# Optimization experiments

Measured on AMD Instinct MI355X. Metric: run time of the kernel, lower is better.

Reference implementation:

```python
import jax, jax.numpy as jnp
import numpy as np

V, D, H, B, M, T, PAD = 32000, 512, 3, 32, 512, 4, 1


def setup_inputs() -> dict:
    key = jax.random.key(0)
    ks = jax.random.split(key, 10)
    def emb_tables(k):
        t = 0.1 * jax.random.normal(k, (H + 1, V, D), jnp.float32)
        return t.at[:, PAD, :].set(0.0)  # padding_idx rows are zero
    C_enc = emb_tables(ks[0])
    C_dec = emb_tables(ks[1])
    gru_w_ih = 0.1 * jax.random.normal(ks[2], (3 * D, D), jnp.float32)
    gru_w_hh = 0.1 * jax.random.normal(ks[3], (3 * D, D), jnp.float32)
    gru_b_ih = jnp.zeros((3 * D,), jnp.float32)
    gru_b_hh = jnp.zeros((3 * D,), jnp.float32)
    W1_w = 0.1 * jax.random.normal(ks[4], (V, 2 * D), jnp.float32)
    W1_b = jnp.zeros((V,), jnp.float32)
    story = jax.random.randint(ks[5], (B, M, T), 0, V, jnp.int32)
    enc_query = jax.random.randint(ks[6], (B,), 0, V, jnp.int32)
    return {"story": story, "enc_query": enc_query, "C_enc": C_enc,
            "C_dec": C_dec, "gru_w_ih": gru_w_ih, "gru_w_hh": gru_w_hh,
            "gru_b_ih": gru_b_ih, "gru_b_hh": gru_b_hh, "W1_w": W1_w,
            "W1_b": W1_b}


def _mem_embed(table, story):
    # table [V, D], story [B, M, T] -> sum-pooled memory [B, M, D]
    return jnp.sum(table[story], axis=2)


def _forward(C_enc, C_dec, gru_w_ih, gru_w_hh, gru_b_ih, gru_b_hh,
             W1_w, W1_b, story, enc_query):
    # ---- EncoderMemNN.forward (eval mode, no unk_mask dropout) ----
    u = jnp.zeros((story.shape[0], D), C_enc.dtype)
    for hop in range(H):
        m_A = _mem_embed(C_enc[hop], story)            # [B, M, D]
        prob = jax.nn.softmax(jnp.einsum('bmd,bd->bm', m_A, u), axis=1)
        m_C = _mem_embed(C_enc[hop + 1], story)        # [B, M, D]
        u = u + jnp.einsum('bmd,bm->bd', m_C, prob)
    enc_hidden = u                                     # decoder_hidden[0]

    # ---- DecoderrMemNN.ptrMemDecoder: single GRU step ----
    x = C_dec[0][enc_query]                            # [B, D]
    gi = x @ gru_w_ih.T + gru_b_ih                     # [B, 3D]
    gh = enc_hidden @ gru_w_hh.T + gru_b_hh            # [B, 3D]
    i_r, i_z, i_n = jnp.split(gi, 3, axis=1)
    h_r, h_z, h_n = jnp.split(gh, 3, axis=1)
    r = jax.nn.sigmoid(i_r + h_r)
    z = jax.nn.sigmoid(i_z + h_z)
    n = jnp.tanh(i_n + r * h_n)
    hidden = (1.0 - z) * n + z * enc_hidden            # new GRU hidden [B, D]

    # ---- DecoderrMemNN.load_memory: m_story[h] = sum-pooled C_dec[h] ----
    m_story = [_mem_embed(C_dec[h], story) for h in range(H + 1)]

    # ---- multi-hop pointer attention ----
    u0 = hidden
    uk = hidden
    p_vocab = None
    for hop in range(H):
        prob_lg = jnp.einsum('bmd,bd->bm', m_story[hop], uk)   # [B, M]
        prob = jax.nn.softmax(prob_lg, axis=1)
        o_k = jnp.einsum('bmd,bm->bd', m_story[hop + 1], prob)  # [B, D]
        if hop == 0:
            p_vocab = jnp.concatenate([u0, o_k], axis=1) @ W1_w.T + W1_b
        uk = uk + o_k
    p_ptr = prob_lg                                    # logits from last hop
    return p_ptr, p_vocab, hidden[None]                # hidden [1, B, D]


def reference(story, enc_query, C_enc, C_dec, gru_w_ih, gru_w_hh,
              gru_b_ih, gru_b_hh, W1_w, W1_b):
    return _forward(C_enc, C_dec, gru_w_ih, gru_w_hh, gru_b_ih, gru_b_hh,
                    W1_w, W1_b, story, enc_query)
```

## Files before the change

kernel.cpp:

```cpp
#include <hip/hip_runtime.h>
#include <math.h>

#define DD 512
#define MM 512
#define BB 32
#define TT 4
#define VV 32000

__global__ __launch_bounds__(256) void poolwsum_kernel(const float* __restrict__ table,
                                                       const int* __restrict__ story,
                                                       const float* __restrict__ s,
                                                       float* __restrict__ partial) {
  __shared__ float wsh[16];
  __shared__ int rows[64];
  __shared__ float red[16];
  int b = blockIdx.x >> 5;
  int c = blockIdx.x & 31;
  int t = threadIdx.x;
  if (s) {
    float v0 = s[b * MM + t], v1 = s[b * MM + t + 256];
    float mx = fmaxf(v0, v1);
#pragma unroll
    for (int off = 32; off > 0; off >>= 1) mx = fmaxf(mx, __shfl_xor(mx, off));
    if ((t & 63) == 0) red[t >> 6] = mx;
    __syncthreads();
    mx = fmaxf(fmaxf(red[0], red[1]), fmaxf(red[2], red[3]));
    float e0 = expf(v0 - mx), e1 = expf(v1 - mx);
    float sm = e0 + e1;
#pragma unroll
    for (int off = 32; off > 0; off >>= 1) sm += __shfl_xor(sm, off);
    if ((t & 63) == 0) red[8 + (t >> 6)] = sm;
    __syncthreads();
    sm = red[8] + red[9] + red[10] + red[11];
    float inv = 1.0f / sm;
    if (t < 16) wsh[t] = expf(s[b * MM + c * 16 + t] - mx) * inv;
  } else {
    if (t < 16) wsh[t] = 1.0f / MM;
  }
  if (t < 64) rows[t] = story[((b << 9) + (c << 4)) * TT + t];
  __syncthreads();
  float acc0 = 0.f, acc1 = 0.f;
#pragma unroll 8
  for (int i = 0; i < 64; ++i) {
    const float* r = table + (size_t)rows[i] * DD;
    float wm = wsh[i >> 2];
    acc0 += wm * r[t];
    acc1 += wm * r[t + 256];
  }
  float* pp = partial + (size_t)blockIdx.x * DD;
  pp[t] = acc0;
  pp[t + 256] = acc1;
}

__global__ void wsumB_kernel(const float* __restrict__ partial,
                             const float* __restrict__ prev,
                             float* __restrict__ uout) {
  int i = blockIdx.x * 256 + threadIdx.x;
  int b = i >> 9, d = i & 511;
  float acc = prev ? prev[i] : 0.f;
  const float* pp = partial + (size_t)b * 32 * DD + d;
#pragma unroll
  for (int c = 0; c < 32; ++c) acc += pp[c * DD];
  uout[i] = acc;
}

__global__ void wsumB2_kernel(const float* __restrict__ partial,
                              const float* __restrict__ hid,
                              float* __restrict__ uk, float* __restrict__ hc) {
  int i = blockIdx.x * 256 + threadIdx.x;
  int b = i >> 9, d = i & 511;
  float ov = 0.f;
  const float* pp = partial + (size_t)b * 32 * DD + d;
#pragma unroll
  for (int c = 0; c < 32; ++c) ov += pp[c * DD];
  float hv = hid[i];
  uk[i] = hv + ov;
  hc[b * 1024 + d] = hv;
  hc[b * 1024 + 512 + d] = ov;
}

__global__ __launch_bounds__(256) void pooldot_kernel(const float* __restrict__ table,
                                                      const int* __restrict__ story,
                                                      const float* __restrict__ u,
                                                      float* __restrict__ s) {
  int wave = (blockIdx.x << 2) + (threadIdx.x >> 6);
  int lane = threadIdx.x & 63;
  int b = wave >> 9;
  const int* st = story + wave * TT;
  size_t r0 = (size_t)st[0] * DD, r1 = (size_t)st[1] * DD;
  size_t r2 = (size_t)st[2] * DD, r3 = (size_t)st[3] * DD;
  const float4* t4 = (const float4*)table;
  const float4* ur = (const float4*)(u + (size_t)b * DD);
  float acc = 0.f;
#pragma unroll
  for (int h = 0; h < 2; ++h) {
    int c = (h << 6) + lane;
    float4 a = t4[(r0 >> 2) + c];
    float4 bb = t4[(r1 >> 2) + c];
    float4 cc = t4[(r2 >> 2) + c];
    float4 d = t4[(r3 >> 2) + c];
    float4 q = ur[c];
    acc += (a.x + bb.x + cc.x + d.x) * q.x;
    acc += (a.y + bb.y + cc.y + d.y) * q.y;
    acc += (a.z + bb.z + cc.z + d.z) * q.z;
    acc += (a.w + bb.w + cc.w + d.w) * q.w;
  }
#pragma unroll
  for (int off = 32; off > 0; off >>= 1) acc += __shfl_xor(acc, off);
  if (lane == 0) s[wave] = acc;
}

__global__ __launch_bounds__(256) void matvec_kernel(const float* __restrict__ W,
                                                     const float* __restrict__ bias,
                                                     const float* __restrict__ vin,
                                                     const int* __restrict__ q,
                                                     const float* __restrict__ table,
                                                     float* __restrict__ out) {
  int idx = (blockIdx.x << 2) + (threadIdx.x >> 6);
  int lane = threadIdx.x & 63;
  int b = idx / 1536;
  int j = idx - b * 1536;
  const float* xb = vin ? (vin + (size_t)b * DD) : (table + (size_t)q[b] * DD);
  const float4* Wr = (const float4*)(W + (size_t)j * DD);
  const float4* xr = (const float4*)xb;
  float acc = 0.f;
#pragma unroll
  for (int h = 0; h < 2; ++h) {
    int c = (h << 6) + lane;
    float4 a = Wr[c];
    float4 qv = xr[c];
    acc += a.x * qv.x + a.y * qv.y + a.z * qv.z + a.w * qv.w;
  }
#pragma unroll
  for (int off = 32; off > 0; off >>= 1) acc += __shfl_xor(acc, off);
  if (lane == 0) out[idx] = acc + bias[j];
}

__global__ void gate_kernel(const float* __restrict__ gi, const float* __restrict__ gh,
                            const float* __restrict__ u, float* __restrict__ hidden,
                            float* __restrict__ out_h) {
  int i = blockIdx.x * 256 + threadIdx.x;
  int b = i >> 9, d = i & 511;
  const float* gib = gi + b * 1536;
  const float* ghb = gh + b * 1536;
  float i_r = gib[d], i_z = gib[d + 512], i_n = gib[d + 1024];
  float h_r = ghb[d], h_z = ghb[d + 512], h_n = ghb[d + 1024];
  float r = 1.f / (1.f + expf(-(i_r + h_r)));
  float z = 1.f / (1.f + expf(-(i_z + h_z)));
  float n = tanhf(i_n + r * h_n);
  float h = (1.f - z) * n + z * u[i];
  hidden[i] = h;
  out_h[i] = h;
}

__global__ __launch_bounds__(256) void pvocab_kernel(const float* __restrict__ Hcat,
                                                     const float* __restrict__ W1,
                                                     const float* __restrict__ W1b,
                                                     float* __restrict__ out) {
  __shared__ float As[32][36];
  __shared__ float Bs[32][68];
  int t = threadIdx.x;
  int v0 = blockIdx.x * 64;
  int tb = t >> 5;
  int tv = t & 31;
  int br = t >> 2;
  int bk = (t & 3) << 3;
  const float* Wp = W1 + (size_t)(v0 + br) * 1024 + bk;
  int ab = t >> 3;
  int ak = (t & 7) << 2;
  const float* Ap = Hcat + (size_t)ab * 1024 + ak;

  float acc[4][2] = {{0.f, 0.f}, {0.f, 0.f}, {0.f, 0.f}, {0.f, 0.f}};

  float4 aReg = *(const float4*)(Ap);
  float4 wReg0 = *(const float4*)(Wp);
  float4 wReg1 = *(const float4*)(Wp + 4);

  for (int k0 = 0; k0 < 1024; k0 += 32) {
    As[ak + 0][ab] = aReg.x; As[ak + 1][ab] = aReg.y;
    As[ak + 2][ab] = aReg.z; As[ak + 3][ab] = aReg.w;
    Bs[bk + 0][br] = wReg0.x; Bs[bk + 1][br] = wReg0.y;
    Bs[bk + 2][br] = wReg0.z; Bs[bk + 3][br] = wReg0.w;
    Bs[bk + 4][br] = wReg1.x; Bs[bk + 5][br] = wReg1.y;
    Bs[bk + 6][br] = wReg1.z; Bs[bk + 7][br] = wReg1.w;
    __syncthreads();
    if (k0 + 32 < 1024) {
      aReg = *(const float4*)(Ap + k0 + 32);
      wReg0 = *(const float4*)(Wp + k0 + 32);
      wReg1 = *(const float4*)(Wp + k0 + 36);
    }
#pragma unroll
    for (int k = 0; k < 32; ++k) {
      float2 bv = *(const float2*)&Bs[k][tv * 2];
      float4 av = *(const float4*)&As[k][tb * 4];
      acc[0][0] += av.x * bv.x; acc[0][1] += av.x * bv.y;
      acc[1][0] += av.y * bv.x; acc[1][1] += av.y * bv.y;
      acc[2][0] += av.z * bv.x; acc[2][1] += av.z * bv.y;
      acc[3][0] += av.w * bv.x; acc[3][1] += av.w * bv.y;
    }
    __syncthreads();
  }
  int v = v0 + tv * 2;
  float b0 = W1b[v], b1 = W1b[v + 1];
#pragma unroll
  for (int i = 0; i < 4; ++i) {
    float2 r;
    r.x = acc[i][0] + b0;
    r.y = acc[i][1] + b1;
    *(float2*)(out + (size_t)(tb * 4 + i) * VV + v) = r;
  }
}

extern "C" void kernel_launch(void* const* d_in, const int* in_sizes, int n_in,
                              void* d_out, int out_size, void* d_ws, size_t ws_size,
                              hipStream_t stream) {
  const int* story = (const int*)d_in[0];
  const int* q = (const int*)d_in[1];
  const float* C_enc = (const float*)d_in[2];
  const float* C_dec = (const float*)d_in[3];
  const float* W_ih = (const float*)d_in[4];
  const float* W_hh = (const float*)d_in[5];
  const float* b_ih = (const float*)d_in[6];
  const float* b_hh = (const float*)d_in[7];
  const float* W1 = (const float*)d_in[8];
  const float* W1b = (const float*)d_in[9];
  float* out = (float*)d_out;

  const size_t VD = (size_t)VV * DD;
  const float* C1 = C_enc + 1 * VD;
  const float* C2 = C_enc + 2 * VD;
  const float* C3 = C_enc + 3 * VD;
  const float* D0 = C_dec + 0 * VD;
  const float* D1 = C_dec + 1 * VD;
  const float* D2 = C_dec + 2 * VD;

  float* part = (float*)d_ws;
  float* u = part + (size_t)BB * 32 * DD;
  float* s = u + BB * DD;
  float* gi = s + BB * MM;
  float* gh = gi + BB * 3 * DD;
  float* hid = gh + BB * 3 * DD;
  float* uk = hid + BB * DD;
  float* hc = uk + BB * DD;

  float* p_ptr_out = out;
  float* p_vocab_out = out + BB * MM;
  float* hid_out = out + BB * MM + (size_t)BB * VV;

  dim3 blk(256);
  const int pwGrid = BB * 32;
  const int pdGrid = BB * MM / 4;
  const int mvGrid = BB * 3 * DD / 4;
  const int ewGrid = BB * DD / 256;

  poolwsum_kernel<<<pwGrid, blk, 0, stream>>>(C1, story, nullptr, part);
  wsumB_kernel<<<ewGrid, blk, 0, stream>>>(part, nullptr, u);
  pooldot_kernel<<<pdGrid, blk, 0, stream>>>(C1, story, u, s);
  poolwsum_kernel<<<pwGrid, blk, 0, stream>>>(C2, story, s, part);
  wsumB_kernel<<<ewGrid, blk, 0, stream>>>(part, u, u);
  pooldot_kernel<<<pdGrid, blk, 0, stream>>>(C2, story, u, s);
  poolwsum_kernel<<<pwGrid, blk, 0, stream>>>(C3, story, s, part);
  wsumB_kernel<<<ewGrid, blk, 0, stream>>>(part, u, u);

  matvec_kernel<<<mvGrid, blk, 0, stream>>>(W_ih, b_ih, nullptr, q, C_dec, gi);
  matvec_kernel<<<mvGrid, blk, 0, stream>>>(W_hh, b_hh, u, nullptr, nullptr, gh);
  gate_kernel<<<ewGrid, blk, 0, stream>>>(gi, gh, u, hid, hid_out);

  pooldot_kernel<<<pdGrid, blk, 0, stream>>>(D0, story, hid, s);
  poolwsum_kernel<<<pwGrid, blk, 0, stream>>>(D1, story, s, part);
  wsumB2_kernel<<<ewGrid, blk, 0, stream>>>(part, hid, uk, hc);
  pooldot_kernel<<<pdGrid, blk, 0, stream>>>(D1, story, uk, s);
  poolwsum_kernel<<<pwGrid, blk, 0, stream>>>(D2, story, s, part);
  wsumB_kernel<<<ewGrid, blk, 0, stream>>>(part, uk, uk);
  pooldot_kernel<<<pdGrid, blk, 0, stream>>>(D2, story, uk, p_ptr_out);

  pvocab_kernel<<<VV / 64, blk, 0, stream>>>(hc, W1, W1b, p_vocab_out);
}
```

Before: 297.7 us.

## Replace gathered pool-dot with dense vocab dot product plus index gather

Instead of gathering four table rows per memory slot and dotting each with the query, the code computes the query against every vocabulary row as a small tiled GEMM, then sums four scalar lookups per slot. This turns random 2KB row gathers (about twice the table size per call) into a single coalesced streaming pass over the table. It adds a 32x32000 intermediate buffer and an extra kernel launch per hop, and the GEMM grid of 500 blocks may leave some CUs idle.

```diff
diff --git a/kernel.cpp b/kernel.cpp
--- a/kernel.cpp
+++ b/kernel.cpp
@@ -79,35 +79,70 @@
   hc[b * 1024 + 512 + d] = ov;
 }
 
-__global__ __launch_bounds__(256) void pooldot_kernel(const float* __restrict__ table,
-                                                      const int* __restrict__ story,
-                                                      const float* __restrict__ u,
-                                                      float* __restrict__ s) {
-  int wave = (blockIdx.x << 2) + (threadIdx.x >> 6);
-  int lane = threadIdx.x & 63;
-  int b = wave >> 9;
-  const int* st = story + wave * TT;
-  size_t r0 = (size_t)st[0] * DD, r1 = (size_t)st[1] * DD;
-  size_t r2 = (size_t)st[2] * DD, r3 = (size_t)st[3] * DD;
-  const float4* t4 = (const float4*)table;
-  const float4* ur = (const float4*)(u + (size_t)b * DD);
-  float acc = 0.f;
-#pragma unroll
-  for (int h = 0; h < 2; ++h) {
-    int c = (h << 6) + lane;
-    float4 a = t4[(r0 >> 2) + c];
-    float4 bb = t4[(r1 >> 2) + c];
-    float4 cc = t4[(r2 >> 2) + c];
-    float4 d = t4[(r3 >> 2) + c];
-    float4 q = ur[c];
-    acc += (a.x + bb.x + cc.x + d.x) * q.x;
-    acc += (a.y + bb.y + cc.y + d.y) * q.y;
-    acc += (a.z + bb.z + cc.z + d.z) * q.z;
-    acc += (a.w + bb.w + cc.w + d.w) * q.w;
-  }
-#pragma unroll
-  for (int off = 32; off > 0; off >>= 1) acc += __shfl_xor(acc, off);
-  if (lane == 0) s[wave] = acc;
+__global__ __launch_bounds__(256) void dotV_kernel(const float* __restrict__ u,
+                                                   const float* __restrict__ C,
+                                                   float* __restrict__ dotv) {
+  __shared__ float As[32][36];
+  __shared__ float Bs[32][68];
+  int t = threadIdx.x;
+  int v0 = blockIdx.x * 64;
+  int tb = t >> 5;
+  int tv = t & 31;
+  int br = t >> 2;
+  int bk = (t & 3) << 3;
+  const float* Wp = C + (size_t)(v0 + br) * DD + bk;
+  int ab = t >> 3;
+  int ak = (t & 7) << 2;
+  const float* Ap = u + (size_t)ab * DD + ak;
+
+  float acc[4][2] = {{0.f, 0.f}, {0.f, 0.f}, {0.f, 0.f}, {0.f, 0.f}};
+
+  float4 aReg = *(const float4*)(Ap);
+  float4 wReg0 = *(const float4*)(Wp);
+  float4 wReg1 = *(const float4*)(Wp + 4);
+
+  for (int k0 = 0; k0 < DD; k0 += 32) {
+    As[ak + 0][ab] = aReg.x; As[ak + 1][ab] = aReg.y;
+    As[ak + 2][ab] = aReg.z; As[ak + 3][ab] = aReg.w;
+    Bs[bk + 0][br] = wReg0.x; Bs[bk + 1][br] = wReg0.y;
+    Bs[bk + 2][br] = wReg0.z; Bs[bk + 3][br] = wReg0.w;
+    Bs[bk + 4][br] = wReg1.x; Bs[bk + 5][br] = wReg1.y;
+    Bs[bk + 6][br] = wReg1.z; Bs[bk + 7][br] = wReg1.w;
+    __syncthreads();
+    if (k0 + 32 < DD) {
+      aReg = *(const float4*)(Ap + k0 + 32);
+      wReg0 = *(const float4*)(Wp + k0 + 32);
+      wReg1 = *(const float4*)(Wp + k0 + 36);
+    }
+#pragma unroll
+    for (int k = 0; k < 32; ++k) {
+      float2 bv = *(const float2*)&Bs[k][tv * 2];
+      float4 av = *(const float4*)&As[k][tb * 4];
+      acc[0][0] += av.x * bv.x; acc[0][1] += av.x * bv.y;
+      acc[1][0] += av.y * bv.x; acc[1][1] += av.y * bv.y;
+      acc[2][0] += av.z * bv.x; acc[2][1] += av.z * bv.y;
+      acc[3][0] += av.w * bv.x; acc[3][1] += av.w * bv.y;
+    }
+    __syncthreads();
+  }
+  int v = v0 + tv * 2;
+#pragma unroll
+  for (int i = 0; i < 4; ++i) {
+    float2 r;
+    r.x = acc[i][0];
+    r.y = acc[i][1];
+    *(float2*)(dotv + (size_t)(tb * 4 + i) * VV + v) = r;
+  }
+}
+
+__global__ void gatherS_kernel(const float* __restrict__ dotv,
+                               const int* __restrict__ story,
+                               float* __restrict__ out) {
+  int i = blockIdx.x * 256 + threadIdx.x;
+  int b = i >> 9;
+  const float* dv = dotv + (size_t)b * VV;
+  int4 ix = *(const int4*)(story + (size_t)i * 4);
+  out[i] = dv[ix.x] + dv[ix.y] + dv[ix.z] + dv[ix.w];
 }
 
 __global__ __launch_bounds__(256) void matvec_kernel(const float* __restrict__ W,
@@ -235,7 +270,8 @@
   const float* D2 = C_dec + 2 * VD;
 
   float* part = (float*)d_ws;
-  float* u = part + (size_t)BB * 32 * DD;
+  float* dotv = part + (size_t)BB * 32 * DD;
+  float* u = dotv + (size_t)BB * VV;
   float* s = u + BB * DD;
   float* gi = s + BB * MM;
   float* gh = gi + BB * 3 * DD;
@@ -249,16 +285,17 @@
 
   dim3 blk(256);
   const int pwGrid = BB * 32;
-  const int pdGrid = BB * MM / 4;
   const int mvGrid = BB * 3 * DD / 4;
   const int ewGrid = BB * DD / 256;
 
   poolwsum_kernel<<<pwGrid, blk, 0, stream>>>(C1, story, nullptr, part);
   wsumB_kernel<<<ewGrid, blk, 0, stream>>>(part, nullptr, u);
-  pooldot_kernel<<<pdGrid, blk, 0, stream>>>(C1, story, u, s);
+  dotV_kernel<<<VV / 64, blk, 0, stream>>>(u, C1, dotv);
+  gatherS_kernel<<<ewGrid, blk, 0, stream>>>(dotv, story, s);
   poolwsum_kernel<<<pwGrid, blk, 0, stream>>>(C2, story, s, part);
   wsumB_kernel<<<ewGrid, blk, 0, stream>>>(part, u, u);
-  pooldot_kernel<<<pdGrid, blk, 0, stream>>>(C2, story, u, s);
+  dotV_kernel<<<VV / 64, blk, 0, stream>>>(u, C2, dotv);
+  gatherS_kernel<<<ewGrid, blk, 0, stream>>>(dotv, story, s);
   poolwsum_kernel<<<pwGrid, blk, 0, stream>>>(C3, story, s, part);
   wsumB_kernel<<<ewGrid, blk, 0, stream>>>(part, u, u);
 
@@ -266,13 +303,16 @@
   matvec_kernel<<<mvGrid, blk, 0, stream>>>(W_hh, b_hh, u, nullptr, nullptr, gh);
   gate_kernel<<<ewGrid, blk, 0, stream>>>(gi, gh, u, hid, hid_out);
 
-  pooldot_kernel<<<pdGrid, blk, 0, stream>>>(D0, story, hid, s);
+  dotV_kernel<<<VV / 64, blk, 0, stream>>>(hid, D0, dotv);
+  gatherS_kernel<<<ewGrid, blk, 0, stream>>>(dotv, story, s);
   poolwsum_kernel<<<pwGrid, blk, 0, stream>>>(D1, story, s, part);
   wsumB2_kernel<<<ewGrid, blk, 0, stream>>>(part, hid, uk, hc);
-  pooldot_kernel<<<pdGrid, blk, 0, stream>>>(D1, story, uk, s);
+  dotV_kernel<<<VV / 64, blk, 0, stream>>>(uk, D1, dotv);
+  gatherS_kernel<<<ewGrid, blk, 0, stream>>>(dotv, story, s);
   poolwsum_kernel<<<pwGrid, blk, 0, stream>>>(D2, story, s, part);
   wsumB_kernel<<<ewGrid, blk, 0, stream>>>(part, uk, uk);
-  pooldot_kernel<<<pdGrid, blk, 0, stream>>>(D2, story, uk, p_ptr_out);
+  dotV_kernel<<<VV / 64, blk, 0, stream>>>(uk, D2, dotv);
+  gatherS_kernel<<<ewGrid, blk, 0, stream>>>(dotv, story, p_ptr_out);
 
   pvocab_kernel<<<VV / 64, blk, 0, stream>>>(hc, W1, W1b, p_vocab_out);
 }
```

Measured after the change: 370.5 us. +24.4%, slower.
